# Optimization experiments

Measured on AMD Instinct MI355X. Metric: run time of the kernel, lower is better.

The kernel has to match this reference:

```python
import jax, jax.numpy as jnp
import numpy as np

# module hyper-params (init_kwargs); shift_sz=1 => 1x1 patches == pixels, flag == mask
SHIFT_SZ = 1
STRIDE = 1
MASK_THRED = 1
TRIPLE_WEIGHT = 1.0   # only rescales gradients in the original custom backward; forward output unchanged
FUSE = True
FUSE_K = 3            # contextual-attention fuse kernel size (identity 3x3)


def _fuse_scores(score, H, W):
    # score: [B, L, L] (query loc, key loc). Contextual-attention 'fuse':
    # smooth the score map with an identity kernel along both spatial unfoldings.
    B, L, _ = score.shape
    eye = jnp.eye(FUSE_K, dtype=score.dtype).reshape(1, 1, FUSE_K, FUSE_K)

    def conv(x):
        return jax.lax.conv_general_dilated(
            x, eye, window_strides=(1, 1), padding='SAME',
            dimension_numbers=('NCHW', 'OIHW', 'NCHW'))

    s = conv(score[:, None])                                            # [B,1,L,L]
    s = s.reshape(B, H, W, H, W).transpose(0, 2, 1, 4, 3).reshape(B, 1, L, L)
    s = conv(s)
    s = s.reshape(B, W, H, W, H).transpose(0, 2, 1, 4, 3).reshape(B, L, L)
    return s


def reference(x, mask):
    # x: [B, 2c, H, W]; first c channels = former (decoder feat), last c = latter (encoder feat)
    B, C2, H, W = x.shape
    c = C2 // 2
    L = H * W
    former = x[:, :c]
    latter = x[:, c:]

    # flag: True = inside hole. With shift_sz=1, stride=1, mask_thred=1 the patch flag is the mask itself.
    flag = mask.reshape(L) > 0.5                                        # [L]

    lat = latter.reshape(B, c, L)
    # normalize context (key) patches to unit L2 norm -> cosine-style correlation
    key = lat / jnp.maximum(jnp.linalg.norm(lat, axis=1, keepdims=True), 1e-4)
    score = jnp.einsum('bcl,bck->blk', lat, key)                        # [B, L(query), L(key)]
    if FUSE:
        score = _fuse_scores(score, H, W)

    # only attend to context patches OUTSIDE the hole
    score = jnp.where(flag[None, None, :], -jnp.inf, score)
    attn = jax.nn.softmax(score, axis=-1)                               # [B, L, L]

    # soft shift: attention-weighted gather of former (decoder) features from context pixels
    shift = jnp.einsum('blk,bck->bcl', attn, former.reshape(B, c, L))   # [B, c, L]
    # the shifted feature only fills hole locations; zero elsewhere
    shift = shift * flag[None, None, :].astype(x.dtype)
    shift = shift.reshape(B, c, H, W)

    return jnp.concatenate([former, latter, shift], axis=1)             # [B, 3c, H, W]


def setup_inputs():
    key = jax.random.key(0)
    k1, k2 = jax.random.split(key)
    B, c, H, W = 2, 64, 64, 64
    x = jax.random.normal(k1, (B, 2 * c, H, W), dtype=jnp.float32)
    mask = (jax.random.uniform(k2, (1, 1, H, W)) > 0.75).astype(jnp.float32)
    return {"x": x, "mask": mask}
```

## Files before the change

kernel.cpp:

```cpp
#include <hip/hip_runtime.h>
#include <math.h>


#define L 4096

typedef unsigned int   u32;
typedef unsigned short u16;
typedef short  short8 __attribute__((ext_vector_type(8)));
typedef float  f32x4  __attribute__((ext_vector_type(4)));

#define MFMA(a, b, c) __builtin_amdgcn_mfma_f32_16x16x32_bf16((a), (b), (c), 0, 0, 0)

__device__ __forceinline__ u16 f2bf(float f) {
    u32 u = __float_as_uint(f);
    u32 r = (u + 0x7FFFu + ((u >> 16) & 1u)) >> 16;
    return (u16)r;
}

#define OFF_LATB  0u
#define OFF_KNB   1048576u
#define OFF_FORB  2097152u
#define OFF_FBITS 3145728u
#define OFF_ROWS  3146240u
#define OFF_CNT   3162624u
#define OFF_PART  3211264u

__global__ void k_prep(const float4* __restrict__ x4, float4* __restrict__ out4,
                       u32* __restrict__ fbits, int* __restrict__ cnt)
{
    int i = blockIdx.x * 256 + threadIdx.x;
    if (i < 262144) {
        int b = i >> 17, j = i & 131071;
        out4[b * 196608 + j] = x4[b * 131072 + j];
    } else if (i < 393216) {
        int z = i - 262144; int b = z >> 16, j = z & 65535;
        out4[b * 196608 + 131072 + j] = make_float4(0.f, 0.f, 0.f, 0.f);
    } else if (i < 393344) {
        fbits[i - 393216] = 0u;
    } else if (i == 393344) {
        cnt[0] = 0;
    }
}

__global__ void k_norm(const float* __restrict__ x, u16* __restrict__ latb,
                       u16* __restrict__ knb, u16* __restrict__ forb)
{
    int tid = blockIdx.x * 256 + threadIdx.x;
    int b = tid >> 12, l = tid & 4095;
    const float* xb = x + (size_t)b * 524288;
    float v[64]; float ss = 0.f;
    #pragma unroll
    for (int c = 0; c < 64; ++c) { v[c] = xb[(64 + c) * 4096 + l]; ss += v[c] * v[c]; }
    float inv = 1.f / fmaxf(sqrtf(ss), 1e-4f);
    u16* lr = latb + (size_t)(b * 4096 + l) * 64;
    u16* kr = knb  + (size_t)(b * 4096 + l) * 64;
    #pragma unroll
    for (int c8 = 0; c8 < 8; ++c8) {
        uint4 pl, pk;
        u32 wl[4], wk[4];
        #pragma unroll
        for (int i = 0; i < 4; ++i) {
            float a = v[c8 * 8 + 2 * i], bb2 = v[c8 * 8 + 2 * i + 1];
            wl[i] = (u32)f2bf(a) | ((u32)f2bf(bb2) << 16);
            wk[i] = (u32)f2bf(a * inv) | ((u32)f2bf(bb2 * inv) << 16);
        }
        pl.x = wl[0]; pl.y = wl[1]; pl.z = wl[2]; pl.w = wl[3];
        pk.x = wk[0]; pk.y = wk[1]; pk.z = wk[2]; pk.w = wk[3];
        *(uint4*)(lr + c8 * 8) = pl;
        *(uint4*)(kr + c8 * 8) = pk;
    }
    u16* fr = forb + (size_t)(b * 4096 + l) * 64;
    #pragma unroll
    for (int c8 = 0; c8 < 8; ++c8) {
        u32 wf[4];
        #pragma unroll
        for (int i = 0; i < 4; ++i) {
            float a = xb[(c8 * 8 + 2 * i) * 4096 + l];
            float bb2 = xb[(c8 * 8 + 2 * i + 1) * 4096 + l];
            wf[i] = (u32)f2bf(a) | ((u32)f2bf(bb2) << 16);
        }
        uint4 pf; pf.x = wf[0]; pf.y = wf[1]; pf.z = wf[2]; pf.w = wf[3];
        *(uint4*)(fr + c8 * 8) = pf;
    }
}

__global__ void k_compact(const float* __restrict__ mask, int* __restrict__ rows,
                          int* __restrict__ cnt, u32* __restrict__ fbits)
{
    int l = blockIdx.x * 256 + threadIdx.x;
    if (l >= L) return;
    if (mask[l] > 0.5f) {
        int p = atomicAdd(cnt, 1); rows[p] = l;
        int kp = ((l & 63) << 6) | (l >> 6);
        atomicOr(&fbits[kp >> 5], 1u << (kp & 31));
    }
}

__global__ __launch_bounds__(256, 2)
void k_flash(const u16* __restrict__ latb, const u16* __restrict__ knb,
             const u16* __restrict__ forb, const u32* __restrict__ fbits,
             const int* __restrict__ rows, const int* __restrict__ cnt,
             char* __restrict__ part)
{
    __shared__ __align__(16) char smem[66688];
    const int t = threadIdx.x;
    const int rt = blockIdx.x, ks = blockIdx.y, b = blockIdx.z;
    const int count = cnt[0];
    const int base = rt * 32;
    if (base >= count) return;
    const int nact = min(32, count - base);

    u16*   g_s   = (u16*)(smem);
    u16*   u_s   = (u16*)(smem + 18432);
    u16*   p_s   = (u16*)(smem + 55808);
    float* fac_s = (float*)(smem + 66048);
    int*   rl_s  = (int*)(smem + 66560);

    if (t < 32) rl_s[t] = rows[base + min(t, nact - 1)];
    __syncthreads();

    const size_t boff = (size_t)b * 4096 * 64;

    #pragma unroll
    for (int j = 0; j < 9; ++j) {
        int id = t + 256 * j;
        int r = id / 72, rem = id - r * 72;
        int tap = rem >> 3, c8 = rem & 7;
        int bb = tap / 3, aa = tap - 3 * bb;
        int l = rl_s[r];
        int tl = ((l & 63) << 6) | (l >> 6);
        int mp = tl + bb - 1;
        uint4 val = make_uint4(0, 0, 0, 0);
        if (mp >= 0 && mp < L) {
            int q = (((mp & 63) << 6) | (mp >> 6)) + aa - 1;
            if (q >= 0 && q < L)
                val = *(const uint4*)(latb + boff + (size_t)q * 64 + c8 * 8);
        }
        *(uint4*)(u_s + r * 584 + tap * 64 + c8 * 8) = val;
    }

    const int ln = t & 15, g = (t >> 4) & 3, w = t >> 6;
    float mrun[2] = {-INFINITY, -INFINITY}, srun[2] = {0.f, 0.f};
    f32x4 acc[2][4];
    #pragma unroll
    for (int i = 0; i < 2; ++i)
        #pragma unroll
        for (int jx = 0; jx < 4; ++jx) acc[i][jx] = (f32x4){0.f, 0.f, 0.f, 0.f};

    const int kp0 = ks * 512;
    for (int kt = 0; kt < 4; ++kt) {
        const int k0p = kp0 + kt * 128;
        f32x4 sc[2][2];
        #pragma unroll
        for (int i = 0; i < 2; ++i)
            #pragma unroll
            for (int jx = 0; jx < 2; ++jx) sc[i][jx] = (f32x4){0.f, 0.f, 0.f, 0.f};

        for (int tap = 0; tap < 9; ++tap) {
            const int bb = tap / 3, aa = tap - 3 * (tap / 3);
            __syncthreads();
            #pragma unroll
            for (int j = 0; j < 4; ++j) {
                int id = t + 256 * j;
                int col = id >> 3, c8 = id & 7;
                int mp = k0p + col + bb - 1;
                uint4 val = make_uint4(0, 0, 0, 0);
                if (mp >= 0 && mp < L) {
                    int q = (((mp & 63) << 6) | (mp >> 6)) + aa - 1;
                    if (q >= 0 && q < L)
                        val = *(const uint4*)(knb + boff + (size_t)q * 64 + c8 * 8);
                }
                *(uint4*)(g_s + col * 72 + c8 * 8) = val;
            }
            __syncthreads();
            #pragma unroll
            for (int Ksi = 0; Ksi < 2; ++Ksi) {
                short8 bu0 = *(const short8*)(u_s + ln * 584        + tap * 64 + Ksi * 32 + g * 8);
                short8 bu1 = *(const short8*)(u_s + (16 + ln) * 584 + tap * 64 + Ksi * 32 + g * 8);
                short8 ag0 = *(const short8*)(g_s + (w * 32 + ln) * 72      + Ksi * 32 + g * 8);
                short8 ag1 = *(const short8*)(g_s + (w * 32 + 16 + ln) * 72 + Ksi * 32 + g * 8);
                sc[0][0] = MFMA(ag0, bu0, sc[0][0]);
                sc[0][1] = MFMA(ag0, bu1, sc[0][1]);
                sc[1][0] = MFMA(ag1, bu0, sc[1][0]);
                sc[1][1] = MFMA(ag1, bu1, sc[1][1]);
            }
        }
        __syncthreads();

        u32 bits = fbits[(k0p >> 5) + w];
        #pragma unroll
        for (int Tn = 0; Tn < 2; ++Tn) {
            float sv[2][4]; float mx = -INFINITY;
            #pragma unroll
            for (int Mt = 0; Mt < 2; ++Mt)
                #pragma unroll
                for (int jj = 0; jj < 4; ++jj) {
                    float s = sc[Mt][Tn][jj];
                    if ((bits >> (Mt * 16 + g * 4 + jj)) & 1) s = -INFINITY;
                    sv[Mt][jj] = s; mx = fmaxf(mx, s);
                }
            mx = fmaxf(mx, __shfl_xor(mx, 16));
            mx = fmaxf(mx, __shfl_xor(mx, 32));
            float newm = fmaxf(mrun[Tn], mx);
            float fac, tsum = 0.f;
            u16 pbv[2][4];
            if (newm > -INFINITY) {
                fac = __expf(mrun[Tn] - newm);
                #pragma unroll
                for (int Mt = 0; Mt < 2; ++Mt)
                    #pragma unroll
                    for (int jj = 0; jj < 4; ++jj) {
                        float p = __expf(sv[Mt][jj] - newm);
                        tsum += p; pbv[Mt][jj] = f2bf(p);
                    }
            } else {
                fac = 1.f;
                #pragma unroll
                for (int Mt = 0; Mt < 2; ++Mt)
                    #pragma unroll
                    for (int jj = 0; jj < 4; ++jj) pbv[Mt][jj] = 0;
            }
            tsum += __shfl_xor(tsum, 16);
            tsum += __shfl_xor(tsum, 32);
            srun[Tn] = srun[Tn] * fac + tsum;
            mrun[Tn] = newm;
            #pragma unroll
            for (int Mt = 0; Mt < 2; ++Mt) {
                uint2 pw;
                pw.x = (u32)pbv[Mt][0] | ((u32)pbv[Mt][1] << 16);
                pw.y = (u32)pbv[Mt][2] | ((u32)pbv[Mt][3] << 16);
                *(uint2*)(p_s + w * 1280 + (Tn * 16 + ln) * 40 + Mt * 16 + g * 4) = pw;
            }
            if (g == 0) fac_s[w * 32 + Tn * 16 + ln] = fac;
        }

        {
            u16* F_s = g_s;
            int cp = t & 63, chq = t >> 6;
            int kpA = k0p + 2 * cp, kpB = kpA + 1;
            int kA = ((kpA & 63) << 6) | (kpA >> 6);
            int kB = ((kpB & 63) << 6) | (kpB >> 6);
            const u32* pa = (const u32*)(forb + boff + (size_t)kA * 64 + chq * 16);
            const u32* pc = (const u32*)(forb + boff + (size_t)kB * 64 + chq * 16);
            uint4 A0 = *(const uint4*)pa, A1 = *(const uint4*)(pa + 4);
            uint4 B0 = *(const uint4*)pc, B1 = *(const uint4*)(pc + 4);
            u32 av[8] = {A0.x, A0.y, A0.z, A0.w, A1.x, A1.y, A1.z, A1.w};
            u32 bv[8] = {B0.x, B0.y, B0.z, B0.w, B1.x, B1.y, B1.z, B1.w};
            #pragma unroll
            for (int i = 0; i < 8; ++i) {
                u32 w0 = (av[i] & 0xffffu) | (bv[i] << 16);
                u32 w1 = (av[i] >> 16) | (bv[i] & 0xffff0000u);
                *(u32*)((char*)F_s + (chq * 16 + 2 * i) * 272 + cp * 4) = w0;
                *(u32*)((char*)F_s + (chq * 16 + 2 * i + 1) * 272 + cp * 4) = w1;
            }
        }
        __syncthreads();

        #pragma unroll
        for (int Ml = 0; Ml < 2; ++Ml) {
            f32x4 fr = *(f32x4*)(fac_s + w * 32 + Ml * 16 + g * 4);
            #pragma unroll
            for (int ct = 0; ct < 4; ++ct)
                #pragma unroll
                for (int jj = 0; jj < 4; ++jj)
                    acc[Ml][ct][jj] *= fr[jj];
        }
        short8 pa0 = *(const short8*)(p_s + w * 1280 + ln * 40 + g * 8);
        short8 pa1 = *(const short8*)(p_s + w * 1280 + (16 + ln) * 40 + g * 8);
        #pragma unroll
        for (int ct = 0; ct < 4; ++ct) {
            short8 fb = *(const short8*)(g_s + (ct * 16 + ln) * 136 + w * 32 + g * 8);
            acc[0][ct] = MFMA(pa0, fb, acc[0][ct]);
            acc[1][ct] = MFMA(pa1, fb, acc[1][ct]);
        }
    }

    __syncthreads();
    float* um = (float*)u_s;
    if (g == 0) {
        #pragma unroll
        for (int Tn = 0; Tn < 2; ++Tn) {
            um[(w * 32 + Tn * 16 + ln) * 66 + 0] = mrun[Tn];
            um[(w * 32 + Tn * 16 + ln) * 66 + 1] = srun[Tn];
        }
    }
    #pragma unroll
    for (int Ml = 0; Ml < 2; ++Ml)
        #pragma unroll
        for (int ct = 0; ct < 4; ++ct)
            #pragma unroll
            for (int jj = 0; jj < 4; ++jj)
                um[(w * 32 + Ml * 16 + g * 4 + jj) * 66 + 2 + ct * 16 + ln] = acc[Ml][ct][jj];
    __syncthreads();
    {
        int row = t >> 3, cq = t & 7;
        float m4[4], s4[4];
        #pragma unroll
        for (int wv = 0; wv < 4; ++wv) {
            m4[wv] = um[(wv * 32 + row) * 66];
            s4[wv] = um[(wv * 32 + row) * 66 + 1];
        }
        float M = fmaxf(fmaxf(m4[0], m4[1]), fmaxf(m4[2], m4[3]));
        float S = 0.f; float wx[4];
        if (M > -INFINITY) {
            #pragma unroll
            for (int wv = 0; wv < 4; ++wv) { wx[wv] = __expf(m4[wv] - M); S += s4[wv] * wx[wv]; }
        } else {
            wx[0] = wx[1] = wx[2] = wx[3] = 0.f;
        }
        char* pp = part + ((size_t)((b * 128 + rt) * 8 + ks)) * 4608 + row * 144;
        u16 h[8];
        #pragma unroll
        for (int i = 0; i < 8; ++i) {
            int ch = cq * 8 + i;
            float v = 0.f;
            #pragma unroll
            for (int wv = 0; wv < 4; ++wv) v += wx[wv] * um[(wv * 32 + row) * 66 + 2 + ch];
            h[i] = f2bf(v);
        }
        if (cq == 0) { *(float*)pp = M; *(float*)(pp + 4) = S; }
        uint4 hw;
        hw.x = (u32)h[0] | ((u32)h[1] << 16); hw.y = (u32)h[2] | ((u32)h[3] << 16);
        hw.z = (u32)h[4] | ((u32)h[5] << 16); hw.w = (u32)h[6] | ((u32)h[7] << 16);
        *(uint4*)(pp + 16 + cq * 16) = hw;
    }
}

__global__ void k_reduce(const int* __restrict__ rows, const int* __restrict__ cnt,
                         const char* __restrict__ part, float* __restrict__ out)
{
    int t = threadIdx.x;
    int row = t >> 3, cq = t & 7;
    int rt = blockIdx.x, b = blockIdx.y;
    int count = cnt[0];
    int slot = rt * 32 + row;
    if (slot >= count) return;
    int l = rows[slot];
    const char* pb = part + ((size_t)((b * 128 + rt) * 8)) * 4608 + row * 144;
    float M = -INFINITY, m8[8], s8[8];
    #pragma unroll
    for (int k = 0; k < 8; ++k) {
        m8[k] = *(const float*)(pb + k * 4608);
        s8[k] = *(const float*)(pb + k * 4608 + 4);
        M = fmaxf(M, m8[k]);
    }
    if (!(M > -INFINITY)) return;
    float S = 0.f; float accv[8] = {0.f, 0.f, 0.f, 0.f, 0.f, 0.f, 0.f, 0.f};
    #pragma unroll
    for (int k = 0; k < 8; ++k) {
        float wxv = __expf(m8[k] - M);
        S += s8[k] * wxv;
        uint4 hv = *(const uint4*)(pb + k * 4608 + 16 + cq * 16);
        u32 uu[4] = {hv.x, hv.y, hv.z, hv.w};
        #pragma unroll
        for (int i = 0; i < 4; ++i) {
            accv[2 * i]     += wxv * __uint_as_float((uu[i] & 0xffffu) << 16);
            accv[2 * i + 1] += wxv * __uint_as_float(uu[i] & 0xffff0000u);
        }
    }
    float inv = (S > 0.f) ? 1.f / S : 0.f;
    float* ob = out + (size_t)b * 786432 + 524288 + l;
    #pragma unroll
    for (int i = 0; i < 8; ++i) ob[(size_t)(cq * 8 + i) * 4096] = accv[i] * inv;
}

extern "C" void kernel_launch(void* const* d_in, const int* in_sizes, int n_in,
                              void* d_out, int out_size, void* d_ws, size_t ws_size,
                              hipStream_t stream)
{
    const float* x    = (const float*)d_in[0];
    const float* mask = (const float*)d_in[1];
    float* out = (float*)d_out;
    char* ws = (char*)d_ws;

    u16* latb = (u16*)(ws + OFF_LATB);
    u16* knb  = (u16*)(ws + OFF_KNB);
    u16* forb = (u16*)(ws + OFF_FORB);
    u32* fbits = (u32*)(ws + OFF_FBITS);
    int* rows  = (int*)(ws + OFF_ROWS);
    int* cnt   = (int*)(ws + OFF_CNT);
    char* part = ws + OFF_PART;

    k_prep<<<1537, 256, 0, stream>>>((const float4*)x, (float4*)out, fbits, cnt);
    k_compact<<<16, 256, 0, stream>>>(mask, rows, cnt, fbits);
    k_norm<<<32, 256, 0, stream>>>(x, latb, knb, forb);
    k_flash<<<dim3(128, 8, 2), 256, 0, stream>>>(latb, knb, forb, fbits, rows, cnt, part);
    k_reduce<<<dim3(128, 2), 256, 0, stream>>>(rows, cnt, part, out);
}
```

Baseline: 166.1 us.

## Precompute swizzled 3-tap key array, use 32x32 MFMA with register-resident queries

The setup kernels are merged into one launch, and a new pass precomputes a per-position array of the three horizontally shifted normalized keys, XOR-swizzled for LDS. The flash kernel now loads each 128-key tile once with async global-to-LDS copies instead of rebuilding the tile for each of the nine taps with syncs in between. It also keeps the query taps in registers and switches to 32x32x16 bf16 MFMA. The cost is an extra preprocessing kernel, more workspace (the key buffer aliases the partials region), and higher register and LDS use per block.

```diff
diff --git a/kernel.cpp b/kernel.cpp
--- a/kernel.cpp
+++ b/kernel.cpp
@@ -7,9 +7,9 @@
 typedef unsigned int   u32;
 typedef unsigned short u16;
 typedef short  short8 __attribute__((ext_vector_type(8)));
-typedef float  f32x4  __attribute__((ext_vector_type(4)));
-
-#define MFMA(a, b, c) __builtin_amdgcn_mfma_f32_16x16x32_bf16((a), (b), (c), 0, 0, 0)
+typedef float  f32x16 __attribute__((ext_vector_type(16)));
+
+#define MFMA32(a, b, c) __builtin_amdgcn_mfma_f32_32x32x16_bf16((a), (b), (c), 0, 0, 0)
 
 __device__ __forceinline__ u16 f2bf(float f) {
     u32 u = __float_as_uint(f);
@@ -17,280 +17,276 @@
     return (u16)r;
 }
 
+__device__ __forceinline__ void lds_async16(void* lds, const void* g) {
+    __builtin_amdgcn_global_load_lds((const __attribute__((address_space(1))) u32*)g,
+                                     (__attribute__((address_space(3))) u32*)lds, 16, 0, 0);
+}
+
 #define OFF_LATB  0u
-#define OFF_KNB   1048576u
-#define OFF_FORB  2097152u
-#define OFF_FBITS 3145728u
-#define OFF_ROWS  3146240u
-#define OFF_CNT   3162624u
-#define OFF_PART  3211264u
-
-__global__ void k_prep(const float4* __restrict__ x4, float4* __restrict__ out4,
-                       u32* __restrict__ fbits, int* __restrict__ cnt)
-{
-    int i = blockIdx.x * 256 + threadIdx.x;
-    if (i < 262144) {
-        int b = i >> 17, j = i & 131071;
-        out4[b * 196608 + j] = x4[b * 131072 + j];
-    } else if (i < 393216) {
-        int z = i - 262144; int b = z >> 16, j = z & 65535;
-        out4[b * 196608 + 131072 + j] = make_float4(0.f, 0.f, 0.f, 0.f);
-    } else if (i < 393344) {
-        fbits[i - 393216] = 0u;
-    } else if (i == 393344) {
-        cnt[0] = 0;
-    }
-}
-
-__global__ void k_norm(const float* __restrict__ x, u16* __restrict__ latb,
-                       u16* __restrict__ knb, u16* __restrict__ forb)
+#define OFF_FORB  1048576u
+#define OFF_GARR  2097152u
+#define GARR_BB   1575936u
+#define OFF_FBITS 5249024u
+#define OFF_ROWS  5249536u
+#define OFF_CNT   5265920u
+#define OFF_PART  5266432u
+#define OFF_KNB   5266432u
+
+__global__ void k_pre1(const float4* __restrict__ x4, float4* __restrict__ out4,
+                       const float* __restrict__ x, const float* __restrict__ mask,
+                       u16* __restrict__ latb, u16* __restrict__ knb, u16* __restrict__ forb,
+                       int* __restrict__ rows, int* __restrict__ cnt, u32* __restrict__ fbits)
+{
+    const int blk = blockIdx.x, t = threadIdx.x;
+    if (blk < 1537) {
+        int i = blk * 256 + t;
+        if (i < 262144) {
+            int b = i >> 17, j = i & 131071;
+            out4[b * 196608 + j] = x4[b * 131072 + j];
+        } else if (i < 393216) {
+            int z = i - 262144; int b = z >> 16, j = z & 65535;
+            out4[b * 196608 + 131072 + j] = make_float4(0.f, 0.f, 0.f, 0.f);
+        }
+    } else if (blk < 1569) {
+        int tid = (blk - 1537) * 256 + t;
+        int b = tid >> 12, l = tid & 4095;
+        const float* xb = x + (size_t)b * 524288;
+        float v[64]; float ss = 0.f;
+        #pragma unroll
+        for (int c = 0; c < 64; ++c) { v[c] = xb[(64 + c) * 4096 + l]; ss += v[c] * v[c]; }
+        float inv = 1.f / fmaxf(sqrtf(ss), 1e-4f);
+        u16* lr = latb + (size_t)(b * 4096 + l) * 64;
+        u16* kr = knb  + (size_t)(b * 4096 + l) * 64;
+        #pragma unroll
+        for (int c8 = 0; c8 < 8; ++c8) {
+            u32 wl[4], wk[4];
+            #pragma unroll
+            for (int i = 0; i < 4; ++i) {
+                float a = v[c8 * 8 + 2 * i], bb2 = v[c8 * 8 + 2 * i + 1];
+                wl[i] = (u32)f2bf(a) | ((u32)f2bf(bb2) << 16);
+                wk[i] = (u32)f2bf(a * inv) | ((u32)f2bf(bb2 * inv) << 16);
+            }
+            uint4 pl = make_uint4(wl[0], wl[1], wl[2], wl[3]);
+            uint4 pk = make_uint4(wk[0], wk[1], wk[2], wk[3]);
+            *(uint4*)(lr + c8 * 8) = pl;
+            *(uint4*)(kr + c8 * 8) = pk;
+        }
+        u16* fr = forb + (size_t)(b * 4096 + l) * 64;
+        #pragma unroll
+        for (int c8 = 0; c8 < 8; ++c8) {
+            u32 wf[4];
+            #pragma unroll
+            for (int i = 0; i < 4; ++i) {
+                float a = xb[(c8 * 8 + 2 * i) * 4096 + l];
+                float bb2 = xb[(c8 * 8 + 2 * i + 1) * 4096 + l];
+                wf[i] = (u32)f2bf(a) | ((u32)f2bf(bb2) << 16);
+            }
+            uint4 pf = make_uint4(wf[0], wf[1], wf[2], wf[3]);
+            *(uint4*)(fr + c8 * 8) = pf;
+        }
+    } else {
+        __shared__ int lcnt;
+        __shared__ u32 lb[128];
+        if (t == 0) lcnt = 0;
+        if (t < 128) lb[t] = 0u;
+        __syncthreads();
+        for (int i = t; i < L; i += 256) {
+            if (mask[i] > 0.5f) {
+                int p = atomicAdd(&lcnt, 1); rows[p] = i;
+                int kp = ((i & 63) << 6) | (i >> 6);
+                atomicOr(&lb[kp >> 5], 1u << (kp & 31));
+            }
+        }
+        __syncthreads();
+        if (t < 128) fbits[t] = lb[t];
+        if (t == 0) cnt[0] = lcnt;
+    }
+}
+
+__global__ void k_garr(const u16* __restrict__ knb, char* __restrict__ garr)
 {
     int tid = blockIdx.x * 256 + threadIdx.x;
-    int b = tid >> 12, l = tid & 4095;
-    const float* xb = x + (size_t)b * 524288;
-    float v[64]; float ss = 0.f;
-    #pragma unroll
-    for (int c = 0; c < 64; ++c) { v[c] = xb[(64 + c) * 4096 + l]; ss += v[c] * v[c]; }
-    float inv = 1.f / fmaxf(sqrtf(ss), 1e-4f);
-    u16* lr = latb + (size_t)(b * 4096 + l) * 64;
-    u16* kr = knb  + (size_t)(b * 4096 + l) * 64;
+    if (tid >= 2 * 4104 * 3) return;
+    int b = tid / 12312; int rem = tid - b * 12312;
+    int sg = rem / 3, aa = rem - 3 * (rem / 3);
+    int mp = sg - 1;
+    char* dst = garr + (size_t)b * GARR_BB + (size_t)sg * 384;
+    int key = (sg & 7) << 4;
+    const u16* src = nullptr;
+    if (mp >= 0 && mp < L) {
+        int q = (((mp & 63) << 6) | (mp >> 6)) + aa - 1;
+        if (q >= 0 && q < L) src = knb + (size_t)b * 262144 + (size_t)q * 64;
+    }
     #pragma unroll
     for (int c8 = 0; c8 < 8; ++c8) {
-        uint4 pl, pk;
-        u32 wl[4], wk[4];
-        #pragma unroll
-        for (int i = 0; i < 4; ++i) {
-            float a = v[c8 * 8 + 2 * i], bb2 = v[c8 * 8 + 2 * i + 1];
-            wl[i] = (u32)f2bf(a) | ((u32)f2bf(bb2) << 16);
-            wk[i] = (u32)f2bf(a * inv) | ((u32)f2bf(bb2 * inv) << 16);
-        }
-        pl.x = wl[0]; pl.y = wl[1]; pl.z = wl[2]; pl.w = wl[3];
-        pk.x = wk[0]; pk.y = wk[1]; pk.z = wk[2]; pk.w = wk[3];
-        *(uint4*)(lr + c8 * 8) = pl;
-        *(uint4*)(kr + c8 * 8) = pk;
-    }
-    u16* fr = forb + (size_t)(b * 4096 + l) * 64;
-    #pragma unroll
-    for (int c8 = 0; c8 < 8; ++c8) {
-        u32 wf[4];
-        #pragma unroll
-        for (int i = 0; i < 4; ++i) {
-            float a = xb[(c8 * 8 + 2 * i) * 4096 + l];
-            float bb2 = xb[(c8 * 8 + 2 * i + 1) * 4096 + l];
-            wf[i] = (u32)f2bf(a) | ((u32)f2bf(bb2) << 16);
-        }
-        uint4 pf; pf.x = wf[0]; pf.y = wf[1]; pf.z = wf[2]; pf.w = wf[3];
-        *(uint4*)(fr + c8 * 8) = pf;
-    }
-}
-
-__global__ void k_compact(const float* __restrict__ mask, int* __restrict__ rows,
-                          int* __restrict__ cnt, u32* __restrict__ fbits)
-{
-    int l = blockIdx.x * 256 + threadIdx.x;
-    if (l >= L) return;
-    if (mask[l] > 0.5f) {
-        int p = atomicAdd(cnt, 1); rows[p] = l;
-        int kp = ((l & 63) << 6) | (l >> 6);
-        atomicOr(&fbits[kp >> 5], 1u << (kp & 31));
+        uint4 v = src ? *(const uint4*)(src + c8 * 8) : make_uint4(0, 0, 0, 0);
+        *(uint4*)(dst + ((aa * 128 + c8 * 16) ^ key)) = v;
     }
 }
 
 __global__ __launch_bounds__(256, 2)
-void k_flash(const u16* __restrict__ latb, const u16* __restrict__ knb,
-             const u16* __restrict__ forb, const u32* __restrict__ fbits,
+void k_flash(const u16* __restrict__ latb, const u16* __restrict__ forb,
+             const char* __restrict__ garr, const u32* __restrict__ fbits,
              const int* __restrict__ rows, const int* __restrict__ cnt,
              char* __restrict__ part)
 {
-    __shared__ __align__(16) char smem[66688];
+    __shared__ __align__(16) char smem[80000];
+    char* slab = smem;
+    u16*  F_s  = (u16*)(smem + 52224);
+    u16*  p_s  = (u16*)(smem + 69632);
+    int*  rl_s = (int*)(smem + 79872);
+
     const int t = threadIdx.x;
     const int rt = blockIdx.x, ks = blockIdx.y, b = blockIdx.z;
     const int count = cnt[0];
     const int base = rt * 32;
     if (base >= count) return;
     const int nact = min(32, count - base);
-
-    u16*   g_s   = (u16*)(smem);
-    u16*   u_s   = (u16*)(smem + 18432);
-    u16*   p_s   = (u16*)(smem + 55808);
-    float* fac_s = (float*)(smem + 66048);
-    int*   rl_s  = (int*)(smem + 66560);
-
     if (t < 32) rl_s[t] = rows[base + min(t, nact - 1)];
     __syncthreads();
 
-    const size_t boff = (size_t)b * 4096 * 64;
-
-    #pragma unroll
-    for (int j = 0; j < 9; ++j) {
-        int id = t + 256 * j;
-        int r = id / 72, rem = id - r * 72;
-        int tap = rem >> 3, c8 = rem & 7;
-        int bb = tap / 3, aa = tap - 3 * bb;
-        int l = rl_s[r];
-        int tl = ((l & 63) << 6) | (l >> 6);
-        int mp = tl + bb - 1;
-        uint4 val = make_uint4(0, 0, 0, 0);
+    const int l = t & 63, w = t >> 6;
+    const int li = l & 31, hi = l >> 5;
+    const size_t boff = (size_t)b * 262144;
+
+    const u16* zp = (const u16*)garr;
+    int gl = rl_s[li];
+    int tl0 = ((gl & 63) << 6) | (gl >> 6);
+    const u16* rp[9];
+    #pragma unroll
+    for (int tap = 0; tap < 9; ++tap) {
+        int bb = tap / 3, aa = tap - 3 * (tap / 3);
+        int mp = tl0 + bb - 1;
+        const u16* p = zp;
         if (mp >= 0 && mp < L) {
             int q = (((mp & 63) << 6) | (mp >> 6)) + aa - 1;
-            if (q >= 0 && q < L)
-                val = *(const uint4*)(latb + boff + (size_t)q * 64 + c8 * 8);
-        }
-        *(uint4*)(u_s + r * 584 + tap * 64 + c8 * 8) = val;
-    }
-
-    const int ln = t & 15, g = (t >> 4) & 3, w = t >> 6;
-    float mrun[2] = {-INFINITY, -INFINITY}, srun[2] = {0.f, 0.f};
-    f32x4 acc[2][4];
-    #pragma unroll
-    for (int i = 0; i < 2; ++i)
-        #pragma unroll
-        for (int jx = 0; jx < 4; ++jx) acc[i][jx] = (f32x4){0.f, 0.f, 0.f, 0.f};
+            if (q >= 0 && q < L) p = latb + boff + (size_t)q * 64;
+        }
+        rp[tap] = p;
+    }
+    short8 bu[36];
+    #pragma unroll
+    for (int q = 0; q < 36; ++q) {
+        int tap = q >> 2, Ksi = q & 3;
+        bu[q] = *(const short8*)(rp[tap] + Ksi * 16 + hi * 8);
+    }
+
+    float mrun = -INFINITY, srun = 0.f;
+    f32x16 acc0, acc1;
+    #pragma unroll
+    for (int r = 0; r < 16; ++r) { acc0[r] = 0.f; acc1[r] = 0.f; }
 
     const int kp0 = ks * 512;
+    const char* gb = garr + (size_t)b * GARR_BB;
+
     for (int kt = 0; kt < 4; ++kt) {
         const int k0p = kp0 + kt * 128;
-        f32x4 sc[2][2];
-        #pragma unroll
-        for (int i = 0; i < 2; ++i)
-            #pragma unroll
-            for (int jx = 0; jx < 2; ++jx) sc[i][jx] = (f32x4){0.f, 0.f, 0.f, 0.f};
-
-        for (int tap = 0; tap < 9; ++tap) {
-            const int bb = tap / 3, aa = tap - 3 * (tap / 3);
-            __syncthreads();
-            #pragma unroll
-            for (int j = 0; j < 4; ++j) {
-                int id = t + 256 * j;
-                int col = id >> 3, c8 = id & 7;
-                int mp = k0p + col + bb - 1;
-                uint4 val = make_uint4(0, 0, 0, 0);
-                if (mp >= 0 && mp < L) {
-                    int q = (((mp & 63) << 6) | (mp >> 6)) + aa - 1;
-                    if (q >= 0 && q < L)
-                        val = *(const uint4*)(knb + boff + (size_t)q * 64 + c8 * 8);
-                }
-                *(uint4*)(g_s + col * 72 + c8 * 8) = val;
-            }
-            __syncthreads();
-            #pragma unroll
-            for (int Ksi = 0; Ksi < 2; ++Ksi) {
-                short8 bu0 = *(const short8*)(u_s + ln * 584        + tap * 64 + Ksi * 32 + g * 8);
-                short8 bu1 = *(const short8*)(u_s + (16 + ln) * 584 + tap * 64 + Ksi * 32 + g * 8);
-                short8 ag0 = *(const short8*)(g_s + (w * 32 + ln) * 72      + Ksi * 32 + g * 8);
-                short8 ag1 = *(const short8*)(g_s + (w * 32 + 16 + ln) * 72 + Ksi * 32 + g * 8);
-                sc[0][0] = MFMA(ag0, bu0, sc[0][0]);
-                sc[0][1] = MFMA(ag0, bu1, sc[0][1]);
-                sc[1][0] = MFMA(ag1, bu0, sc[1][0]);
-                sc[1][1] = MFMA(ag1, bu1, sc[1][1]);
-            }
-        }
         __syncthreads();
 
-        u32 bits = fbits[(k0p >> 5) + w];
-        #pragma unroll
-        for (int Tn = 0; Tn < 2; ++Tn) {
-            float sv[2][4]; float mx = -INFINITY;
-            #pragma unroll
-            for (int Mt = 0; Mt < 2; ++Mt)
-                #pragma unroll
-                for (int jj = 0; jj < 4; ++jj) {
-                    float s = sc[Mt][Tn][jj];
-                    if ((bits >> (Mt * 16 + g * 4 + jj)) & 1) s = -INFINITY;
-                    sv[Mt][jj] = s; mx = fmaxf(mx, s);
-                }
-            mx = fmaxf(mx, __shfl_xor(mx, 16));
-            mx = fmaxf(mx, __shfl_xor(mx, 32));
-            float newm = fmaxf(mrun[Tn], mx);
-            float fac, tsum = 0.f;
-            u16 pbv[2][4];
-            if (newm > -INFINITY) {
-                fac = __expf(mrun[Tn] - newm);
-                #pragma unroll
-                for (int Mt = 0; Mt < 2; ++Mt)
-                    #pragma unroll
-                    for (int jj = 0; jj < 4; ++jj) {
-                        float p = __expf(sv[Mt][jj] - newm);
-                        tsum += p; pbv[Mt][jj] = f2bf(p);
-                    }
-            } else {
-                fac = 1.f;
-                #pragma unroll
-                for (int Mt = 0; Mt < 2; ++Mt)
-                    #pragma unroll
-                    for (int jj = 0; jj < 4; ++jj) pbv[Mt][jj] = 0;
-            }
-            tsum += __shfl_xor(tsum, 16);
-            tsum += __shfl_xor(tsum, 32);
-            srun[Tn] = srun[Tn] * fac + tsum;
-            mrun[Tn] = newm;
-            #pragma unroll
-            for (int Mt = 0; Mt < 2; ++Mt) {
-                uint2 pw;
-                pw.x = (u32)pbv[Mt][0] | ((u32)pbv[Mt][1] << 16);
-                pw.y = (u32)pbv[Mt][2] | ((u32)pbv[Mt][3] << 16);
-                *(uint2*)(p_s + w * 1280 + (Tn * 16 + ln) * 40 + Mt * 16 + g * 4) = pw;
-            }
-            if (g == 0) fac_s[w * 32 + Tn * 16 + ln] = fac;
+        const char* gw = gb + (size_t)k0p * 384;
+        #pragma unroll
+        for (int i = 0; i < 13; ++i) {
+            int idx = w + 4 * i;
+            if (idx < 51)
+                lds_async16(slab + idx * 1024, gw + idx * 1024 + l * 16);
         }
 
         {
-            u16* F_s = g_s;
-            int cp = t & 63, chq = t >> 6;
-            int kpA = k0p + 2 * cp, kpB = kpA + 1;
+            int kpA = k0p + 2 * l, kpB = kpA + 1;
             int kA = ((kpA & 63) << 6) | (kpA >> 6);
             int kB = ((kpB & 63) << 6) | (kpB >> 6);
-            const u32* pa = (const u32*)(forb + boff + (size_t)kA * 64 + chq * 16);
-            const u32* pc = (const u32*)(forb + boff + (size_t)kB * 64 + chq * 16);
+            const u32* pa = (const u32*)(forb + boff + (size_t)kA * 64 + w * 16);
+            const u32* pc = (const u32*)(forb + boff + (size_t)kB * 64 + w * 16);
             uint4 A0 = *(const uint4*)pa, A1 = *(const uint4*)(pa + 4);
             uint4 B0 = *(const uint4*)pc, B1 = *(const uint4*)(pc + 4);
             u32 av[8] = {A0.x, A0.y, A0.z, A0.w, A1.x, A1.y, A1.z, A1.w};
             u32 bv[8] = {B0.x, B0.y, B0.z, B0.w, B1.x, B1.y, B1.z, B1.w};
             #pragma unroll
-            for (int i = 0; i < 8; ++i) {
-                u32 w0 = (av[i] & 0xffffu) | (bv[i] << 16);
-                u32 w1 = (av[i] >> 16) | (bv[i] & 0xffff0000u);
-                *(u32*)((char*)F_s + (chq * 16 + 2 * i) * 272 + cp * 4) = w0;
-                *(u32*)((char*)F_s + (chq * 16 + 2 * i + 1) * 272 + cp * 4) = w1;
-            }
-        }
+            for (int i2 = 0; i2 < 8; ++i2) {
+                u32 w0 = (av[i2] & 0xffffu) | (bv[i2] << 16);
+                u32 w1 = (av[i2] >> 16) | (bv[i2] & 0xffff0000u);
+                *(u32*)((char*)F_s + (w * 16 + 2 * i2) * 272 + l * 4) = w0;
+                *(u32*)((char*)F_s + (w * 16 + 2 * i2 + 1) * 272 + l * 4) = w1;
+            }
+        }
+        asm volatile("s_waitcnt vmcnt(0)" ::: "memory");
         __syncthreads();
 
-        #pragma unroll
-        for (int Ml = 0; Ml < 2; ++Ml) {
-            f32x4 fr = *(f32x4*)(fac_s + w * 32 + Ml * 16 + g * 4);
-            #pragma unroll
-            for (int ct = 0; ct < 4; ++ct)
-                #pragma unroll
-                for (int jj = 0; jj < 4; ++jj)
-                    acc[Ml][ct][jj] *= fr[jj];
-        }
-        short8 pa0 = *(const short8*)(p_s + w * 1280 + ln * 40 + g * 8);
-        short8 pa1 = *(const short8*)(p_s + w * 1280 + (16 + ln) * 40 + g * 8);
-        #pragma unroll
-        for (int ct = 0; ct < 4; ++ct) {
-            short8 fb = *(const short8*)(g_s + (ct * 16 + ln) * 136 + w * 32 + g * 8);
-            acc[0][ct] = MFMA(pa0, fb, acc[0][ct]);
-            acc[1][ct] = MFMA(pa1, fb, acc[1][ct]);
+        f32x16 sc;
+        #pragma unroll
+        for (int r = 0; r < 16; ++r) sc[r] = 0.f;
+        const int slot_base = w * 32 + li;
+        #pragma unroll
+        for (int tap = 0; tap < 9; ++tap) {
+            int bb = tap / 3, aa = tap - 3 * (tap / 3);
+            int sl = slot_base + bb;
+            int key = (sl & 7) << 4;
+            int base_b = sl * 384 + aa * 128 + hi * 16;
+            #pragma unroll
+            for (int Ksi = 0; Ksi < 4; ++Ksi) {
+                short8 ag = *(const short8*)(slab + ((base_b + Ksi * 32) ^ key));
+                sc = MFMA32(ag, bu[tap * 4 + Ksi], sc);
+            }
+        }
+
+        u32 bits = fbits[(k0p >> 5) + w];
+        float sv[16]; float mx = -INFINITY;
+        #pragma unroll
+        for (int r = 0; r < 16; ++r) {
+            int kloc = (r & 3) + 8 * (r >> 2) + 4 * hi;
+            float s = sc[r];
+            if ((bits >> kloc) & 1) s = -INFINITY;
+            sv[r] = s; mx = fmaxf(mx, s);
+        }
+        mx = fmaxf(mx, __shfl_xor(mx, 32, 64));
+        float newm = fmaxf(mrun, mx);
+        float fac, tsum = 0.f;
+        u16 pb[16];
+        if (newm > -INFINITY) {
+            fac = __expf(mrun - newm);
+            #pragma unroll
+            for (int r = 0; r < 16; ++r) { float p = __expf(sv[r] - newm); tsum += p; pb[r] = f2bf(p); }
+        } else {
+            fac = 1.f;
+            #pragma unroll
+            for (int r = 0; r < 16; ++r) pb[r] = 0;
+        }
+        tsum += __shfl_xor(tsum, 32, 64);
+        srun = srun * fac + tsum;
+        mrun = newm;
+        #pragma unroll
+        for (int rq = 0; rq < 8; ++rq) {
+            int r = rq * 2;
+            int kloc = (r & 3) + 8 * (r >> 2) + 4 * hi;
+            u32 pw = (u32)pb[r] | ((u32)pb[r + 1] << 16);
+            *(u32*)(p_s + w * 1280 + li * 40 + kloc) = pw;
+        }
+
+        #pragma unroll
+        for (int r = 0; r < 16; ++r) {
+            int row = (r & 3) + 8 * (r >> 2) + 4 * hi;
+            float fr = __shfl(fac, row, 64);
+            acc0[r] *= fr; acc1[r] *= fr;
+        }
+        #pragma unroll
+        for (int Ksi2 = 0; Ksi2 < 2; ++Ksi2) {
+            short8 pa2 = *(const short8*)(p_s + w * 1280 + li * 40 + Ksi2 * 16 + hi * 8);
+            short8 f0 = *(const short8*)(F_s + li * 136 + w * 32 + Ksi2 * 16 + hi * 8);
+            short8 f1 = *(const short8*)(F_s + (32 + li) * 136 + w * 32 + Ksi2 * 16 + hi * 8);
+            acc0 = MFMA32(pa2, f0, acc0);
+            acc1 = MFMA32(pa2, f1, acc1);
         }
     }
 
     __syncthreads();
-    float* um = (float*)u_s;
-    if (g == 0) {
-        #pragma unroll
-        for (int Tn = 0; Tn < 2; ++Tn) {
-            um[(w * 32 + Tn * 16 + ln) * 66 + 0] = mrun[Tn];
-            um[(w * 32 + Tn * 16 + ln) * 66 + 1] = srun[Tn];
-        }
-    }
-    #pragma unroll
-    for (int Ml = 0; Ml < 2; ++Ml)
-        #pragma unroll
-        for (int ct = 0; ct < 4; ++ct)
-            #pragma unroll
-            for (int jj = 0; jj < 4; ++jj)
-                um[(w * 32 + Ml * 16 + g * 4 + jj) * 66 + 2 + ct * 16 + ln] = acc[Ml][ct][jj];
+    float* um = (float*)smem;
+    if (l < 32) { um[(w * 32 + li) * 66] = mrun; um[(w * 32 + li) * 66 + 1] = srun; }
+    #pragma unroll
+    for (int r = 0; r < 16; ++r) {
+        int row = (r & 3) + 8 * (r >> 2) + 4 * hi;
+        um[(w * 32 + row) * 66 + 2 + li] = acc0[r];
+        um[(w * 32 + row) * 66 + 2 + 32 + li] = acc1[r];
+    }
     __syncthreads();
     {
         int row = t >> 3, cq = t & 7;
@@ -374,16 +370,17 @@
     char* ws = (char*)d_ws;
 
     u16* latb = (u16*)(ws + OFF_LATB);
-    u16* knb  = (u16*)(ws + OFF_KNB);
     u16* forb = (u16*)(ws + OFF_FORB);
+    char* garr = ws + OFF_GARR;
     u32* fbits = (u32*)(ws + OFF_FBITS);
     int* rows  = (int*)(ws + OFF_ROWS);
     int* cnt   = (int*)(ws + OFF_CNT);
     char* part = ws + OFF_PART;
-
-    k_prep<<<1537, 256, 0, stream>>>((const float4*)x, (float4*)out, fbits, cnt);
-    k_compact<<<16, 256, 0, stream>>>(mask, rows, cnt, fbits);
-    k_norm<<<32, 256, 0, stream>>>(x, latb, knb, forb);
-    k_flash<<<dim3(128, 8, 2), 256, 0, stream>>>(latb, knb, forb, fbits, rows, cnt, part);
+    u16* knb   = (u16*)(ws + OFF_KNB);
+
+    k_pre1<<<1570, 256, 0, stream>>>((const float4*)x, (float4*)out, x, mask,
+                                     latb, knb, forb, rows, cnt, fbits);
+    k_garr<<<97, 256, 0, stream>>>(knb, garr);
+    k_flash<<<dim3(128, 8, 2), 256, 0, stream>>>(latb, forb, garr, fbits, rows, cnt, part);
     k_reduce<<<dim3(128, 2), 256, 0, stream>>>(rows, cnt, part, out);
 }
```

Measured after the change: 143.7 us. -13.4%, faster.
